# Optimization experiments

Hardware: AMD Instinct MI355X
Metric: run time of the kernel (lower is better)

## Reference

```python
import jax, jax.numpy as jnp
import numpy as np

EPS = 1e-5
NUM_HEADS = 8


def _conv_transpose_3x3_s2(x, w):
    # x: [B,Cin,H,W], w: [Cin,Cout,3,3] (torch ConvTranspose2d layout), stride 2, no padding
    # output spatial = (H-1)*2 + 3 = 2H+1
    return jax.lax.conv_transpose(
        x, w, strides=(2, 2), padding='VALID',
        dimension_numbers=('NCHW', 'IOHW', 'NCHW'))


def setup_inputs() -> dict:
    key = jax.random.key(0)
    ks = jax.random.split(key, 8)
    B, C, H, W = 4, 256, 32, 32
    Co, Dk, Dv = 128, 64, 64
    s = 0.05
    return {
        'x': jax.random.normal(ks[0], (B, C, H, W), jnp.float32),
        'gamma': jnp.ones((C,), jnp.float32),
        'beta': jnp.zeros((C,), jnp.float32),
        'running_mean': jax.random.normal(ks[1], (C,), jnp.float32) * 0.1,
        'running_var': jax.random.uniform(ks[2], (C,), jnp.float32, 0.5, 1.5),
        'w_sc': jax.random.normal(ks[3], (C, Co, 3, 3), jnp.float32) * s,
        'w_q': jax.random.normal(ks[4], (C, Dk, 3, 3), jnp.float32) * s,
        'w_k': jax.random.normal(ks[5], (Dk, C), jnp.float32) * s,
        'w_v': jax.random.normal(ks[6], (Dv, C), jnp.float32) * s,
        'w_o': jax.random.normal(ks[7], (Co, Dv), jnp.float32) * s,
    }


def reference(x, gamma, beta, running_mean, running_var, w_sc, w_q, w_k, w_v, w_o):
    B, C, H, W = x.shape
    h = NUM_HEADS
    # BatchNorm (inference, running stats) + ReLU, shared by both branches
    inv = jax.lax.rsqrt(running_var + EPS)
    xn = (x - running_mean[None, :, None, None]) * (gamma * inv)[None, :, None, None] \
         + beta[None, :, None, None]
    xr = jax.nn.relu(xn)

    # Shortcut: ConvTranspose2d(C->Co, 3, stride 2) -> [B,Co,2H+1,2W+1]
    shortcut = _conv_transpose_3x3_s2(xr, w_sc)

    # Attention branch ('UP'): query upsampled via ConvTranspose, k/v 1x1 at low res
    q = _conv_transpose_3x3_s2(xr, w_q)              # [B,Dk,Hu,Wu]
    k = jnp.einsum('dc,bchw->bdhw', w_k, xr)         # [B,Dk,H,W]
    v = jnp.einsum('dc,bchw->bdhw', w_v, xr)         # [B,Dv,H,W]
    Hu, Wu = q.shape[2], q.shape[3]
    Nq, Nk = Hu * Wu, H * W
    Dk, Dv = q.shape[1], v.shape[1]
    dk = Dk // h
    qh = q.reshape(B, h, dk, Nq)
    kh = k.reshape(B, h, dk, Nk)
    vh = v.reshape(B, h, Dv // h, Nk)
    scores = jnp.einsum('bhdq,bhdk->bhqk', qh, kh) / jnp.sqrt(jnp.float32(dk))
    attn = jax.nn.softmax(scores, axis=-1)           # use_softmax=True
    out = jnp.einsum('bhqk,bhdk->bhdq', attn, vh)    # [B,h,dv,Nq]
    out = out.reshape(B, Dv, Hu, Wu)
    out = jnp.einsum('od,bdhw->bohw', w_o, out)      # 1x1 output projection -> Co

    return shortcut + out
```

## Files before the change

### kernel.cpp

```cpp
#include <hip/hip_runtime.h>

typedef unsigned short u16;
typedef unsigned int u32;

typedef float f4 __attribute__((ext_vector_type(4)));
typedef short s8v __attribute__((ext_vector_type(8)));
typedef u16 us8 __attribute__((ext_vector_type(8)));
typedef _Float16 h4 __attribute__((ext_vector_type(4)));
typedef __fp16 g2 __attribute__((ext_vector_type(2)));

__device__ __forceinline__ u16 f2bf(float x){ u32 b=__float_as_uint(x); b += 0x7FFFu + ((b>>16)&1u); return (u16)(b>>16); }
__device__ __forceinline__ u16 f2h(float x){ union{_Float16 h; u16 u;} c; c.h=(_Float16)x; return c.u; }

#define O_XRT  4096u
#define O_WPT  (O_XRT + 2367488u)
#define O_QH   (O_WPT + 884736u)
#define O_KT   (O_QH  + 2163200u)
#define O_V    (O_KT  + 524288u)
#define O_ATT  (O_V   + 524288u)
#define O_WKV  (O_ATT + 2163200u)
#define O_WO2  (O_WKV + 65536u)

__global__ __launch_bounds__(256) void k_prep(
    const float* __restrict__ x, const float* __restrict__ gamma, const float* __restrict__ beta,
    const float* __restrict__ mean, const float* __restrict__ var,
    const float* __restrict__ w_sc, const float* __restrict__ w_q,
    const float* __restrict__ w_k, const float* __restrict__ w_v, const float* __restrict__ w_o,
    u16* __restrict__ xrTp, u16* __restrict__ wpt,
    u16* __restrict__ wkv, u16* __restrict__ wo2)
{
  __shared__ float SS[128], SH[128];
  __shared__ __align__(16) u16 T[32*136];
  int bi = blockIdx.x, tid = threadIdx.x;
  if (bi < 256) {
    int b = bi >> 6, pt = (bi >> 1) & 31, ch = bi & 1;
    int pix0 = pt*32, c0 = ch*128;
    if (tid < 128) {
      int c = c0 + tid;
      float s = gamma[c]*rsqrtf(var[c] + 1e-5f);
      SS[tid] = s; SH[tid] = beta[c] - mean[c]*s;
    }
    __syncthreads();
    int pix_l = tid & 31, c_l = tid >> 5;
    #pragma unroll 4
    for (int it = 0; it < 16; ++it) {
      int cl = it*8 + c_l;
      float v = x[(((size_t)(b*256 + c0 + cl))<<10) + pix0 + pix_l];
      T[pix_l*136 + cl] = f2bf(fmaxf(v*SS[cl] + SH[cl], 0.f));
    }
    __syncthreads();
    int pix_r = tid >> 3, j = tid & 7;
    us8 v0 = *(const us8*)(T + pix_r*136 + j*8);
    us8 v1 = *(const us8*)(T + pix_r*136 + 64 + j*8);
    u16* dst = xrTp + (((size_t)(b*1156 + (pt+1)*34 + 1 + pix_r))<<8) + c0;
    *(us8*)(dst + j*8) = v0;
    *(us8*)(dst + 64 + j*8) = v1;
    return;
  }
  int wid = (bi - 256)*256 + tid;
  if (wid < 442368) {
    int c, m, ky, kx; float val;
    if (wid < 294912) {
      c = wid / 1152; int r = wid - c*1152; m = r / 9; int t9 = r - m*9; ky = t9/3; kx = t9 - ky*3;
      val = w_sc[wid];
    } else {
      int i2 = wid - 294912;
      c = i2 / 576; int r = i2 - c*576; m = r / 9; int t9 = r - m*9; ky = t9/3; kx = t9 - ky*3;
      val = w_q[i2] * 0.51007023f;
      m += 128;
    }
    int py = (ky==1) ? 1 : 0; int dy = (ky==0) ? 1 : 0;
    int px = (kx==1) ? 1 : 0; int dx = (kx==0) ? 1 : 0;
    int cls = py*2 + px;
    int tt, KP, base;
    if (cls==0){ tt = dy*2+dx; KP=1024; base=0; }
    else if (cls==1){ tt = dy; KP=512; base=196608; }
    else if (cls==2){ tt = dx; KP=512; base=294912; }
    else { tt = 0; KP=256; base=393216; }
    wpt[base + m*KP + tt*256 + c] = f2bf(val);
  } else if (wid < 475136) {
    int i = wid - 442368; int m = i >> 8, c = i & 255;
    float vv = (m < 64) ? w_k[m*256 + c] : w_v[(m-64)*256 + c];
    wkv[m*256 + c] = f2bf(vv);
  } else if (wid < 483328) {
    int i = wid - 475136;
    wo2[i] = f2bf(w_o[i]);
  } else if (wid < 500224) {
    int i = wid - 483328;
    int b = i / 4224; int r = i - b*4224;
    int hp = r >> 5, j = r & 31;
    int p;
    if (hp < 34) p = hp;
    else if (hp < 68) p = 33*34 + (hp - 34);
    else if (hp < 100) p = (hp - 68 + 1)*34;
    else p = (hp - 100 + 1)*34 + 33;
    *(us8*)(xrTp + (((size_t)(b*1156 + p))<<8) + j*8) = (us8)0;
  }
}

template<int PY,int PX,int TT>
__device__ __forceinline__ void conv_cls(
    const u16* __restrict__ xrTp, const u16* __restrict__ wcls,
    float* __restrict__ outF, u16* __restrict__ qh,
    int mb, int nb, u16* Blds)
{
  constexpr int Hy = 33 - PY, Wx = 33 - PX;
  constexpr int NC = 4*Hy*Wx;
  constexpr int KP = TT*256;
  constexpr int NKT = KP/64;
  int tid = threadIdx.x;
  int lane = tid & 63, wv = tid >> 6, quad = lane >> 4, c15 = lane & 15;
  int sn = tid >> 2, sg = tid & 3;
  int n_g = nb*64 + sn;
  int ncl = n_g < NC ? n_g : NC-1;
  int bb = ncl/(Hy*Wx); int rem = ncl - bb*(Hy*Wx); int yq = rem/Wx; int xq = rem - yq*Wx;
  const u16* bsrc = xrTp + (((size_t)(bb*1156 + (yq+1)*34 + xq+1))<<8) + sg*16;
  f4 acc[4];
  #pragma unroll
  for (int i=0;i<4;i++) acc[i] = (f4){0.f,0.f,0.f,0.f};
  const u16* arow = wcls + (size_t)(mb*64 + wv*16 + c15)*KP + quad*8;
  auto loadB = [&](int kt, us8& v0, us8& v1) {
    int tt = kt >> 2, c0 = (kt & 3)*64;
    int dy, dx;
    if (TT==4){ dy = tt>>1; dx = tt&1; }
    else if (TT==2){ if (PX==1){ dy=tt; dx=0; } else { dy=0; dx=tt; } }
    else { dy=0; dx=0; }
    const u16* p = bsrc - (((dy*34+dx))<<8) + c0;
    v0 = *(const us8*)p;
    v1 = *(const us8*)(p+8);
  };
  us8 cv0, cv1; loadB(0, cv0, cv1);
  int pb = 0;
  for (int kt = 0; kt < NKT; ++kt) {
    u16* Bw = Blds + pb*4608;
    *(us8*)(Bw + sn*72 + sg*16) = cv0;
    *(us8*)(Bw + sn*72 + sg*16 + 8) = cv1;
    __syncthreads();
    if (kt + 1 < NKT) loadB(kt+1, cv0, cv1);
    s8v a0 = *(const s8v*)(arow + kt*64);
    s8v a1 = *(const s8v*)(arow + kt*64 + 32);
    #pragma unroll
    for (int t4=0;t4<4;t4++) {
      const u16* br = Blds + pb*4608 + (t4*16 + c15)*72 + quad*8;
      s8v bf0 = *(const s8v*)br;
      s8v bf1 = *(const s8v*)(br + 32);
      acc[t4] = __builtin_amdgcn_mfma_f32_16x16x32_bf16(a0, bf0, acc[t4], 0, 0, 0);
      acc[t4] = __builtin_amdgcn_mfma_f32_16x16x32_bf16(a1, bf1, acc[t4], 0, 0, 0);
    }
    pb ^= 1;
  }
  #pragma unroll
  for (int t4=0;t4<4;t4++) {
    int n2 = nb*64 + t4*16 + c15;
    if (n2 < NC) {
      int bb2 = n2/(Hy*Wx); int rem2 = n2 - bb2*(Hy*Wx); int yq2 = rem2/Wx; int xq2 = rem2 - yq2*Wx;
      int pix = (2*yq2 + PY)*65 + (2*xq2 + PX);
      if (mb < 2) {
        int mrow = mb*64 + wv*16 + quad*4;
        #pragma unroll
        for (int rg=0; rg<4; rg++)
          outF[(size_t)(bb2*128 + mrow + rg)*4225 + pix] = acc[t4][rg];
      } else {
        int dv = wv*16 + quad*4;
        u16 pk[4];
        #pragma unroll
        for (int rg=0; rg<4; rg++) pk[rg] = f2h(acc[t4][rg]);
        *(uint2*)(qh + (((size_t)(bb2*4225 + pix))<<6) + dv) = *(uint2*)pk;
      }
    }
  }
}

__global__ __launch_bounds__(256) void k_conv(
    const u16* __restrict__ xrTp, const u16* __restrict__ wpt, const u16* __restrict__ wkv,
    float* __restrict__ outF, u16* __restrict__ qh,
    u16* __restrict__ kT, u16* __restrict__ vbuf)
{
  __shared__ __align__(16) u16 Blds[2*4608];
  int bi = blockIdx.x;
  if (bi < 795) {
    int mb = bi % 3, cy = bi / 3;
    if (cy < 69)       conv_cls<0,0,4>(xrTp, wpt,          outF, qh, mb, cy,     Blds);
    else if (cy < 135) conv_cls<0,1,2>(xrTp, wpt + 196608, outF, qh, mb, cy-69,  Blds);
    else if (cy < 201) conv_cls<1,0,2>(xrTp, wpt + 294912, outF, qh, mb, cy-135, Blds);
    else               conv_cls<1,1,1>(xrTp, wpt + 393216, outF, qh, mb, cy-201, Blds);
    return;
  }
  int t = bi - 795;
  int mb = t & 1, nb = t >> 1;
  int tid = threadIdx.x;
  int lane = tid & 63, wv = tid >> 6, quad = lane >> 4, c15 = lane & 15;
  int sn = tid >> 2, sg = tid & 3;
  int n_g = nb*64 + sn;
  int b0 = n_g >> 10, pix0 = n_g & 1023, y0 = pix0 >> 5, x0 = pix0 & 31;
  const u16* bsrc = xrTp + (((size_t)(b0*1156 + (y0+1)*34 + x0+1))<<8) + sg*16;
  f4 acc[4];
  #pragma unroll
  for (int i=0;i<4;i++) acc[i] = (f4){0.f,0.f,0.f,0.f};
  const u16* arow = wkv + (size_t)(mb*64 + wv*16 + c15)*256 + quad*8;
  us8 cv0 = *(const us8*)bsrc, cv1 = *(const us8*)(bsrc + 8);
  int pb = 0;
  for (int kt = 0; kt < 4; ++kt) {
    u16* Bw = Blds + pb*4608;
    *(us8*)(Bw + sn*72 + sg*16) = cv0;
    *(us8*)(Bw + sn*72 + sg*16 + 8) = cv1;
    __syncthreads();
    if (kt < 3) { cv0 = *(const us8*)(bsrc + (kt+1)*64); cv1 = *(const us8*)(bsrc + (kt+1)*64 + 8); }
    s8v a0 = *(const s8v*)(arow + kt*64);
    s8v a1 = *(const s8v*)(arow + kt*64 + 32);
    #pragma unroll
    for (int t4=0;t4<4;t4++) {
      const u16* br = Blds + pb*4608 + (t4*16 + c15)*72 + quad*8;
      s8v bf0 = *(const s8v*)br;
      s8v bf1 = *(const s8v*)(br + 32);
      acc[t4] = __builtin_amdgcn_mfma_f32_16x16x32_bf16(a0, bf0, acc[t4], 0, 0, 0);
      acc[t4] = __builtin_amdgcn_mfma_f32_16x16x32_bf16(a1, bf1, acc[t4], 0, 0, 0);
    }
    pb ^= 1;
  }
  int ml = wv*16 + quad*4;
  #pragma unroll
  for (int t4=0;t4<4;t4++) {
    int n2 = nb*64 + t4*16 + c15;
    int b = n2 >> 10, pix = n2 & 1023;
    if (mb == 0) {
      int h = ml >> 3, d0 = ml & 7;
      u16 pk[4];
      #pragma unroll
      for (int rg=0; rg<4; rg++) pk[rg] = f2h(acc[t4][rg]);
      *(uint2*)(kT + ((size_t)(b*8+h)<<13) + pix*8 + d0) = *(uint2*)pk;
    } else {
      #pragma unroll
      for (int rg=0; rg<4; rg++)
        vbuf[(((size_t)(b*64 + ml + rg))<<10) + pix] = f2h(acc[t4][rg]);
    }
  }
}

__global__ __launch_bounds__(256) void k_attn(
    const u16* __restrict__ qh, const u16* __restrict__ kT, const u16* __restrict__ vbuf,
    u16* __restrict__ attT)
{
  __shared__ __align__(16) u16 KL[8192];
  __shared__ __align__(16) u16 VL[9*1032];
  int qt = blockIdx.x, bh = blockIdx.y;
  int b = bh >> 3, h = bh & 7;
  int tid = threadIdx.x, lane = tid & 63, wv = tid >> 6, quad = lane >> 4, c15 = lane & 15;
  {
    const uint4* kg = (const uint4*)(kT + ((size_t)bh << 13));
    for (int i = tid; i < 1024; i += 256) ((uint4*)KL)[i] = kg[i];
    const u16* vg = vbuf + ((size_t)(b*64 + h*8) << 10);
    for (int i = tid; i < 1024; i += 256) {
      int dv = i >> 7, k8 = (i & 127) << 3;
      *(uint4*)(VL + dv*1032 + k8) = *(const uint4*)(vg + (dv<<10) + k8);
    }
    if (tid < 129) {
      us8 ones;
      #pragma unroll
      for (int i=0;i<8;i++) ones[i] = 0x3C00;
      *(us8*)(VL + 8*1032 + tid*8) = ones;
    }
  }
  __syncthreads();
  int q0 = qt*128 + wv*32 + c15;
  int q1 = q0 + 16;
  int qa = q0 < 4224 ? q0 : 4224;
  int qb = q1 < 4224 ? q1 : 4224;
  uint2 t0 = *(const uint2*)(qh + (((size_t)(b*4225 + qa))<<6) + h*8 + (quad&1)*4);
  uint2 t1 = *(const uint2*)(qh + (((size_t)(b*4225 + qb))<<6) + h*8 + (quad&1)*4);
  h4 bq0 = quad < 2 ? *(h4*)&t0 : (h4)(_Float16)0.f;
  h4 bq1 = quad < 2 ? *(h4*)&t1 : (h4)(_Float16)0.f;
  const u16* klb = KL + c15*8 + (quad&1)*4;
  int vr = c15 > 8 ? 8 : c15;
  const u16* vlb = VL + vr*1032 + quad*4;
  const f4 zf = {0.f,0.f,0.f,0.f};
  f4 O0 = {0.f,0.f,0.f,0.f}, O1 = {0.f,0.f,0.f,0.f};
  union HU { uint2 u; h4 h; };
  #pragma unroll 8
  for (int kt=0; kt<64; ++kt) {
    h4 ak = *(const h4*)(klb + kt*128);
    h4 av = *(const h4*)(vlb + kt*16);
    f4 s0 = __builtin_amdgcn_mfma_f32_16x16x16f16(ak, bq0, zf, 0, 0, 0);
    f4 s1 = __builtin_amdgcn_mfma_f32_16x16x16f16(ak, bq1, zf, 0, 0, 0);
    g2 p0l = __builtin_amdgcn_cvt_pkrtz(__builtin_amdgcn_exp2f(s0[0]), __builtin_amdgcn_exp2f(s0[1]));
    g2 p0h = __builtin_amdgcn_cvt_pkrtz(__builtin_amdgcn_exp2f(s0[2]), __builtin_amdgcn_exp2f(s0[3]));
    g2 p1l = __builtin_amdgcn_cvt_pkrtz(__builtin_amdgcn_exp2f(s1[0]), __builtin_amdgcn_exp2f(s1[1]));
    g2 p1h = __builtin_amdgcn_cvt_pkrtz(__builtin_amdgcn_exp2f(s1[2]), __builtin_amdgcn_exp2f(s1[3]));
    HU u0; u0.u.x = __builtin_bit_cast(u32, p0l); u0.u.y = __builtin_bit_cast(u32, p0h);
    HU u1; u1.u.x = __builtin_bit_cast(u32, p1l); u1.u.y = __builtin_bit_cast(u32, p1h);
    O0 = __builtin_amdgcn_mfma_f32_16x16x16f16(av, u0.h, O0, 0, 0, 0);
    O1 = __builtin_amdgcn_mfma_f32_16x16x16f16(av, u1.h, O1, 0, 0, 0);
  }
  float l0 = __shfl(O0[0], 32 + c15, 64);
  float l1 = __shfl(O1[0], 32 + c15, 64);
  float r0 = __builtin_amdgcn_rcpf(l0);
  float r1 = __builtin_amdgcn_rcpf(l1);
  if (quad < 2) {
    if (q0 < 4225) {
      u16 pk[4];
      #pragma unroll
      for (int rg=0;rg<4;rg++) pk[rg] = f2bf(O0[rg]*r0);
      *(uint2*)(attT + (((size_t)(b*4225 + q0))<<6) + h*8 + quad*4) = *(uint2*)pk;
    }
    if (q1 < 4225) {
      u16 pk[4];
      #pragma unroll
      for (int rg=0;rg<4;rg++) pk[rg] = f2bf(O1[rg]*r1);
      *(uint2*)(attT + (((size_t)(b*4225 + q1))<<6) + h*8 + quad*4) = *(uint2*)pk;
    }
  }
}

__global__ __launch_bounds__(256) void k_proj(
    const u16* __restrict__ attT, const u16* __restrict__ wo2, float* __restrict__ outF)
{
  int nbi = blockIdx.x, b = blockIdx.y;
  int tid = threadIdx.x;
  int lane = tid & 63, wv = tid >> 6, quad = lane >> 4, c15 = lane & 15;
  f4 acc[2][4];
  #pragma unroll
  for (int am=0;am<2;am++)
    #pragma unroll
    for (int i=0;i<4;i++) acc[am][i] = (f4){0.f,0.f,0.f,0.f};
  #pragma unroll
  for (int kt = 0; kt < 2; ++kt) {
    s8v a0 = *(const s8v*)(wo2 + (size_t)(wv*32 + c15)*64 + kt*32 + quad*8);
    s8v a1 = *(const s8v*)(wo2 + (size_t)(wv*32 + 16 + c15)*64 + kt*32 + quad*8);
    #pragma unroll
    for (int t4=0;t4<4;t4++) {
      int n = nbi*64 + t4*16 + c15;
      int nc = n < 4224 ? n : 4224;
      s8v bf = *(const s8v*)(attT + (((size_t)(b*4225 + nc))<<6) + kt*32 + quad*8);
      acc[0][t4] = __builtin_amdgcn_mfma_f32_16x16x32_bf16(a0, bf, acc[0][t4], 0, 0, 0);
      acc[1][t4] = __builtin_amdgcn_mfma_f32_16x16x32_bf16(a1, bf, acc[1][t4], 0, 0, 0);
    }
  }
  #pragma unroll
  for (int am=0;am<2;am++) {
    int mrow = wv*32 + am*16 + quad*4;
    #pragma unroll
    for (int t4=0;t4<4;t4++) {
      int n2 = nbi*64 + t4*16 + c15;
      if (n2 < 4225) {
        float* op = outF + (size_t)(b*128 + mrow)*4225 + n2;
        #pragma unroll
        for (int rg=0; rg<4; rg++) op[(size_t)rg*4225] += acc[am][t4][rg];
      }
    }
  }
}

extern "C" void kernel_launch(void* const* d_in, const int* in_sizes, int n_in,
                              void* d_out, int out_size, void* d_ws, size_t ws_size,
                              hipStream_t stream) {
  const float* x     = (const float*)d_in[0];
  const float* gamma = (const float*)d_in[1];
  const float* beta  = (const float*)d_in[2];
  const float* mean  = (const float*)d_in[3];
  const float* var   = (const float*)d_in[4];
  const float* w_sc  = (const float*)d_in[5];
  const float* w_q   = (const float*)d_in[6];
  const float* w_k   = (const float*)d_in[7];
  const float* w_v   = (const float*)d_in[8];
  const float* w_o   = (const float*)d_in[9];
  char* ws = (char*)d_ws;
  u16*   xrTp = (u16*)(ws + O_XRT);
  u16*   wpt  = (u16*)(ws + O_WPT);
  u16*   qhb  = (u16*)(ws + O_QH);
  u16*   kT   = (u16*)(ws + O_KT);
  u16*   vbuf = (u16*)(ws + O_V);
  u16*   attT = (u16*)(ws + O_ATT);
  u16*   wkv  = (u16*)(ws + O_WKV);
  u16*   wo2  = (u16*)(ws + O_WO2);
  float* outF = (float*)d_out;

  k_prep<<<2211, 256, 0, stream>>>(x, gamma, beta, mean, var, w_sc, w_q, w_k, w_v, w_o,
                                   xrTp, wpt, wkv, wo2);
  k_conv<<<923, 256, 0, stream>>>(xrTp, wpt, wkv, outF, qhb, kT, vbuf);
  k_attn<<<dim3(34, 32), 256, 0, stream>>>(qhb, kT, vbuf, attT);
  k_proj<<<dim3(67, 4), 256, 0, stream>>>(attT, wo2, outF);
}
```

Measured before the change: 135.5 us.

## Fuse four kernels into persistent megakernel with global atomic barriers

Replaces the prep, conv, attention and projection launches with a single persistent kernel of 1024 blocks that loops over work units and separates stages with atomic-counter grid barriers, after a memset resets the counters. The goal is to remove launch gaps and the tail between kernels. In exchange it adds spin-wait barrier cost, needs all 1024 blocks co-resident (launch bounds of 4 blocks per CU) or it deadlocks, and may lower per-stage occupancy and parallelism, for example in the attention stage, which has more work units than blocks.

```diff
diff --git a/kernel.cpp b/kernel.cpp
--- a/kernel.cpp
+++ b/kernel.cpp
@@ -21,81 +21,17 @@
 #define O_WKV  (O_ATT + 2163200u)
 #define O_WO2  (O_WKV + 65536u)
 
-__global__ __launch_bounds__(256) void k_prep(
-    const float* __restrict__ x, const float* __restrict__ gamma, const float* __restrict__ beta,
-    const float* __restrict__ mean, const float* __restrict__ var,
-    const float* __restrict__ w_sc, const float* __restrict__ w_q,
-    const float* __restrict__ w_k, const float* __restrict__ w_v, const float* __restrict__ w_o,
-    u16* __restrict__ xrTp, u16* __restrict__ wpt,
-    u16* __restrict__ wkv, u16* __restrict__ wo2)
-{
-  __shared__ float SS[128], SH[128];
-  __shared__ __align__(16) u16 T[32*136];
-  int bi = blockIdx.x, tid = threadIdx.x;
-  if (bi < 256) {
-    int b = bi >> 6, pt = (bi >> 1) & 31, ch = bi & 1;
-    int pix0 = pt*32, c0 = ch*128;
-    if (tid < 128) {
-      int c = c0 + tid;
-      float s = gamma[c]*rsqrtf(var[c] + 1e-5f);
-      SS[tid] = s; SH[tid] = beta[c] - mean[c]*s;
-    }
-    __syncthreads();
-    int pix_l = tid & 31, c_l = tid >> 5;
-    #pragma unroll 4
-    for (int it = 0; it < 16; ++it) {
-      int cl = it*8 + c_l;
-      float v = x[(((size_t)(b*256 + c0 + cl))<<10) + pix0 + pix_l];
-      T[pix_l*136 + cl] = f2bf(fmaxf(v*SS[cl] + SH[cl], 0.f));
-    }
-    __syncthreads();
-    int pix_r = tid >> 3, j = tid & 7;
-    us8 v0 = *(const us8*)(T + pix_r*136 + j*8);
-    us8 v1 = *(const us8*)(T + pix_r*136 + 64 + j*8);
-    u16* dst = xrTp + (((size_t)(b*1156 + (pt+1)*34 + 1 + pix_r))<<8) + c0;
-    *(us8*)(dst + j*8) = v0;
-    *(us8*)(dst + 64 + j*8) = v1;
-    return;
-  }
-  int wid = (bi - 256)*256 + tid;
-  if (wid < 442368) {
-    int c, m, ky, kx; float val;
-    if (wid < 294912) {
-      c = wid / 1152; int r = wid - c*1152; m = r / 9; int t9 = r - m*9; ky = t9/3; kx = t9 - ky*3;
-      val = w_sc[wid];
-    } else {
-      int i2 = wid - 294912;
-      c = i2 / 576; int r = i2 - c*576; m = r / 9; int t9 = r - m*9; ky = t9/3; kx = t9 - ky*3;
-      val = w_q[i2] * 0.51007023f;
-      m += 128;
-    }
-    int py = (ky==1) ? 1 : 0; int dy = (ky==0) ? 1 : 0;
-    int px = (kx==1) ? 1 : 0; int dx = (kx==0) ? 1 : 0;
-    int cls = py*2 + px;
-    int tt, KP, base;
-    if (cls==0){ tt = dy*2+dx; KP=1024; base=0; }
-    else if (cls==1){ tt = dy; KP=512; base=196608; }
-    else if (cls==2){ tt = dx; KP=512; base=294912; }
-    else { tt = 0; KP=256; base=393216; }
-    wpt[base + m*KP + tt*256 + c] = f2bf(val);
-  } else if (wid < 475136) {
-    int i = wid - 442368; int m = i >> 8, c = i & 255;
-    float vv = (m < 64) ? w_k[m*256 + c] : w_v[(m-64)*256 + c];
-    wkv[m*256 + c] = f2bf(vv);
-  } else if (wid < 483328) {
-    int i = wid - 475136;
-    wo2[i] = f2bf(w_o[i]);
-  } else if (wid < 500224) {
-    int i = wid - 483328;
-    int b = i / 4224; int r = i - b*4224;
-    int hp = r >> 5, j = r & 31;
-    int p;
-    if (hp < 34) p = hp;
-    else if (hp < 68) p = 33*34 + (hp - 34);
-    else if (hp < 100) p = (hp - 68 + 1)*34;
-    else p = (hp - 100 + 1)*34 + 33;
-    *(us8*)(xrTp + (((size_t)(b*1156 + p))<<8) + j*8) = (us8)0;
-  }
+#define NBLK 1024
+
+__device__ __forceinline__ void gbar(u32* c) {
+  __syncthreads();
+  if (threadIdx.x == 0) {
+    __threadfence();
+    atomicAdd(c, 1u);
+    while (atomicAdd(c, 0u) < (u32)NBLK) __builtin_amdgcn_s_sleep(4);
+    __threadfence();
+  }
+  __syncthreads();
 }
 
 template<int PY,int PX,int TT>
@@ -171,180 +107,268 @@
   }
 }
 
-__global__ __launch_bounds__(256) void k_conv(
-    const u16* __restrict__ xrTp, const u16* __restrict__ wpt, const u16* __restrict__ wkv,
-    float* __restrict__ outF, u16* __restrict__ qh,
-    u16* __restrict__ kT, u16* __restrict__ vbuf)
+__global__ __launch_bounds__(256, 4) void k_mega(
+    const float* __restrict__ x, const float* __restrict__ gamma, const float* __restrict__ beta,
+    const float* __restrict__ mean, const float* __restrict__ var,
+    const float* __restrict__ w_sc, const float* __restrict__ w_q,
+    const float* __restrict__ w_k, const float* __restrict__ w_v, const float* __restrict__ w_o,
+    char* __restrict__ ws, float* __restrict__ outF)
 {
-  __shared__ __align__(16) u16 Blds[2*4608];
-  int bi = blockIdx.x;
-  if (bi < 795) {
-    int mb = bi % 3, cy = bi / 3;
-    if (cy < 69)       conv_cls<0,0,4>(xrTp, wpt,          outF, qh, mb, cy,     Blds);
-    else if (cy < 135) conv_cls<0,1,2>(xrTp, wpt + 196608, outF, qh, mb, cy-69,  Blds);
-    else if (cy < 201) conv_cls<1,0,2>(xrTp, wpt + 294912, outF, qh, mb, cy-135, Blds);
-    else               conv_cls<1,1,1>(xrTp, wpt + 393216, outF, qh, mb, cy-201, Blds);
-    return;
-  }
-  int t = bi - 795;
-  int mb = t & 1, nb = t >> 1;
-  int tid = threadIdx.x;
-  int lane = tid & 63, wv = tid >> 6, quad = lane >> 4, c15 = lane & 15;
-  int sn = tid >> 2, sg = tid & 3;
-  int n_g = nb*64 + sn;
-  int b0 = n_g >> 10, pix0 = n_g & 1023, y0 = pix0 >> 5, x0 = pix0 & 31;
-  const u16* bsrc = xrTp + (((size_t)(b0*1156 + (y0+1)*34 + x0+1))<<8) + sg*16;
-  f4 acc[4];
-  #pragma unroll
-  for (int i=0;i<4;i++) acc[i] = (f4){0.f,0.f,0.f,0.f};
-  const u16* arow = wkv + (size_t)(mb*64 + wv*16 + c15)*256 + quad*8;
-  us8 cv0 = *(const us8*)bsrc, cv1 = *(const us8*)(bsrc + 8);
-  int pb = 0;
-  for (int kt = 0; kt < 4; ++kt) {
-    u16* Bw = Blds + pb*4608;
-    *(us8*)(Bw + sn*72 + sg*16) = cv0;
-    *(us8*)(Bw + sn*72 + sg*16 + 8) = cv1;
-    __syncthreads();
-    if (kt < 3) { cv0 = *(const us8*)(bsrc + (kt+1)*64); cv1 = *(const us8*)(bsrc + (kt+1)*64 + 8); }
-    s8v a0 = *(const s8v*)(arow + kt*64);
-    s8v a1 = *(const s8v*)(arow + kt*64 + 32);
-    #pragma unroll
-    for (int t4=0;t4<4;t4++) {
-      const u16* br = Blds + pb*4608 + (t4*16 + c15)*72 + quad*8;
-      s8v bf0 = *(const s8v*)br;
-      s8v bf1 = *(const s8v*)(br + 32);
-      acc[t4] = __builtin_amdgcn_mfma_f32_16x16x32_bf16(a0, bf0, acc[t4], 0, 0, 0);
-      acc[t4] = __builtin_amdgcn_mfma_f32_16x16x32_bf16(a1, bf1, acc[t4], 0, 0, 0);
-    }
-    pb ^= 1;
-  }
-  int ml = wv*16 + quad*4;
-  #pragma unroll
-  for (int t4=0;t4<4;t4++) {
-    int n2 = nb*64 + t4*16 + c15;
-    int b = n2 >> 10, pix = n2 & 1023;
-    if (mb == 0) {
-      int h = ml >> 3, d0 = ml & 7;
-      u16 pk[4];
+  __shared__ __align__(16) char SM[35072];
+  u32* bar = (u32*)ws;
+  u16* xrTp = (u16*)(ws + O_XRT);
+  u16* wpt  = (u16*)(ws + O_WPT);
+  u16* qh   = (u16*)(ws + O_QH);
+  u16* kT   = (u16*)(ws + O_KT);
+  u16* vbuf = (u16*)(ws + O_V);
+  u16* attT = (u16*)(ws + O_ATT);
+  u16* wkv  = (u16*)(ws + O_WKV);
+  u16* wo2  = (u16*)(ws + O_WO2);
+  int bid = blockIdx.x, tid = threadIdx.x;
+
+  {
+    float* SS = (float*)SM; float* SH = SS + 64; u16* T = (u16*)(SH + 64);
+    for (int u = bid; u < 2466; u += NBLK) {
+      if (u < 512) {
+        int b = u >> 7, pt = (u >> 2) & 31, ch = u & 3;
+        int pix0 = pt*32, c0 = ch*64;
+        if (tid < 64) {
+          int c = c0 + tid;
+          float s = gamma[c]*rsqrtf(var[c] + 1e-5f);
+          SS[tid] = s; SH[tid] = beta[c] - mean[c]*s;
+        }
+        __syncthreads();
+        int pix_l = tid & 31, c_l = tid >> 5;
+        #pragma unroll
+        for (int it = 0; it < 8; ++it) {
+          int cl = it*8 + c_l;
+          float v = x[(((size_t)(b*256 + c0 + cl))<<10) + pix0 + pix_l];
+          T[pix_l*72 + cl] = f2bf(fmaxf(v*SS[cl] + SH[cl], 0.f));
+        }
+        __syncthreads();
+        int pix_r = tid >> 3, j = tid & 7;
+        us8 v0 = *(const us8*)(T + pix_r*72 + j*8);
+        u16* dst = xrTp + (((size_t)(b*1156 + (pt+1)*34 + 1 + pix_r))<<8) + c0;
+        *(us8*)(dst + j*8) = v0;
+        __syncthreads();
+      } else {
+        int wid = (u - 512)*256 + tid;
+        if (wid < 442368) {
+          int c, m, ky, kx; float val;
+          if (wid < 294912) {
+            c = wid / 1152; int r = wid - c*1152; m = r / 9; int t9 = r - m*9; ky = t9/3; kx = t9 - ky*3;
+            val = w_sc[wid];
+          } else {
+            int i2 = wid - 294912;
+            c = i2 / 576; int r = i2 - c*576; m = r / 9; int t9 = r - m*9; ky = t9/3; kx = t9 - ky*3;
+            val = w_q[i2] * 0.51007023f;
+            m += 128;
+          }
+          int py = (ky==1) ? 1 : 0; int dy = (ky==0) ? 1 : 0;
+          int px = (kx==1) ? 1 : 0; int dx = (kx==0) ? 1 : 0;
+          int cls = py*2 + px;
+          int tt, KP, base;
+          if (cls==0){ tt = dy*2+dx; KP=1024; base=0; }
+          else if (cls==1){ tt = dy; KP=512; base=196608; }
+          else if (cls==2){ tt = dx; KP=512; base=294912; }
+          else { tt = 0; KP=256; base=393216; }
+          wpt[base + m*KP + tt*256 + c] = f2bf(val);
+        } else if (wid < 475136) {
+          int i = wid - 442368; int m = i >> 8, c = i & 255;
+          float vv = (m < 64) ? w_k[m*256 + c] : w_v[(m-64)*256 + c];
+          wkv[m*256 + c] = f2bf(vv);
+        } else if (wid < 483328) {
+          int i = wid - 475136;
+          wo2[i] = f2bf(w_o[i]);
+        } else if (wid < 500224) {
+          int i = wid - 483328;
+          int b = i / 4224; int r = i - b*4224;
+          int hp = r >> 5, j = r & 31;
+          int p;
+          if (hp < 34) p = hp;
+          else if (hp < 68) p = 33*34 + (hp - 34);
+          else if (hp < 100) p = (hp - 68 + 1)*34;
+          else p = (hp - 100 + 1)*34 + 33;
+          *(us8*)(xrTp + (((size_t)(b*1156 + p))<<8) + j*8) = (us8)0;
+        }
+      }
+    }
+  }
+  gbar(bar + 0);
+
+  {
+    u16* Blds = (u16*)SM;
+    for (int u = bid; u < 923; u += NBLK) {
+      if (u < 795) {
+        int mb = u % 3, cy = u / 3;
+        if (cy < 69)       conv_cls<0,0,4>(xrTp, wpt,          outF, qh, mb, cy,     Blds);
+        else if (cy < 135) conv_cls<0,1,2>(xrTp, wpt + 196608, outF, qh, mb, cy-69,  Blds);
+        else if (cy < 201) conv_cls<1,0,2>(xrTp, wpt + 294912, outF, qh, mb, cy-135, Blds);
+        else               conv_cls<1,1,1>(xrTp, wpt + 393216, outF, qh, mb, cy-201, Blds);
+      } else {
+        int t = u - 795;
+        int mb = t & 1, nb = t >> 1;
+        int lane = tid & 63, wv = tid >> 6, quad = lane >> 4, c15 = lane & 15;
+        int sn = tid >> 2, sg = tid & 3;
+        int n_g = nb*64 + sn;
+        int b0 = n_g >> 10, pix0 = n_g & 1023, y0 = pix0 >> 5, x0 = pix0 & 31;
+        const u16* bsrc = xrTp + (((size_t)(b0*1156 + (y0+1)*34 + x0+1))<<8) + sg*16;
+        f4 acc[4];
+        #pragma unroll
+        for (int i=0;i<4;i++) acc[i] = (f4){0.f,0.f,0.f,0.f};
+        const u16* arow = wkv + (size_t)(mb*64 + wv*16 + c15)*256 + quad*8;
+        us8 cv0 = *(const us8*)bsrc, cv1 = *(const us8*)(bsrc + 8);
+        int pb = 0;
+        for (int kt = 0; kt < 4; ++kt) {
+          u16* Bw = Blds + pb*4608;
+          *(us8*)(Bw + sn*72 + sg*16) = cv0;
+          *(us8*)(Bw + sn*72 + sg*16 + 8) = cv1;
+          __syncthreads();
+          if (kt < 3) { cv0 = *(const us8*)(bsrc + (kt+1)*64); cv1 = *(const us8*)(bsrc + (kt+1)*64 + 8); }
+          s8v a0 = *(const s8v*)(arow + kt*64);
+          s8v a1 = *(const s8v*)(arow + kt*64 + 32);
+          #pragma unroll
+          for (int t4=0;t4<4;t4++) {
+            const u16* br = Blds + pb*4608 + (t4*16 + c15)*72 + quad*8;
+            s8v bf0 = *(const s8v*)br;
+            s8v bf1 = *(const s8v*)(br + 32);
+            acc[t4] = __builtin_amdgcn_mfma_f32_16x16x32_bf16(a0, bf0, acc[t4], 0, 0, 0);
+            acc[t4] = __builtin_amdgcn_mfma_f32_16x16x32_bf16(a1, bf1, acc[t4], 0, 0, 0);
+          }
+          pb ^= 1;
+        }
+        int ml = wv*16 + quad*4;
+        #pragma unroll
+        for (int t4=0;t4<4;t4++) {
+          int n2 = nb*64 + t4*16 + c15;
+          int b = n2 >> 10, pix = n2 & 1023;
+          if (mb == 0) {
+            int h = ml >> 3, d0 = ml & 7;
+            u16 pk[4];
+            #pragma unroll
+            for (int rg=0; rg<4; rg++) pk[rg] = f2h(acc[t4][rg]);
+            *(uint2*)(kT + ((size_t)(b*8+h)<<13) + pix*8 + d0) = *(uint2*)pk;
+          } else {
+            #pragma unroll
+            for (int rg=0; rg<4; rg++)
+              vbuf[(((size_t)(b*64 + ml + rg))<<10) + pix] = f2h(acc[t4][rg]);
+          }
+        }
+      }
+      __syncthreads();
+    }
+  }
+  gbar(bar + 1);
+
+  {
+    u16* KL = (u16*)SM;
+    u16* VL = KL + 8192;
+    int lane = tid & 63, wv = tid >> 6, quad = lane >> 4, c15 = lane & 15;
+    for (int u = bid; u < 1088; u += NBLK) {
+      int qt = u % 34, bh = u / 34;
+      int b = bh >> 3, h = bh & 7;
+      {
+        const uint4* kg = (const uint4*)(kT + ((size_t)bh << 13));
+        for (int i = tid; i < 1024; i += 256) ((uint4*)KL)[i] = kg[i];
+        const u16* vg = vbuf + ((size_t)(b*64 + h*8) << 10);
+        for (int i = tid; i < 1024; i += 256) {
+          int dv = i >> 7, k8 = (i & 127) << 3;
+          *(uint4*)(VL + dv*1032 + k8) = *(const uint4*)(vg + (dv<<10) + k8);
+        }
+        if (tid < 129) {
+          us8 ones;
+          #pragma unroll
+          for (int i=0;i<8;i++) ones[i] = 0x3C00;
+          *(us8*)(VL + 8*1032 + tid*8) = ones;
+        }
+      }
+      __syncthreads();
+      int q0 = qt*128 + wv*32 + c15;
+      int q1 = q0 + 16;
+      int qa = q0 < 4224 ? q0 : 4224;
+      int qb = q1 < 4224 ? q1 : 4224;
+      uint2 t0 = *(const uint2*)(qh + (((size_t)(b*4225 + qa))<<6) + h*8 + (quad&1)*4);
+      uint2 t1 = *(const uint2*)(qh + (((size_t)(b*4225 + qb))<<6) + h*8 + (quad&1)*4);
+      h4 bq0 = quad < 2 ? *(h4*)&t0 : (h4)(_Float16)0.f;
+      h4 bq1 = quad < 2 ? *(h4*)&t1 : (h4)(_Float16)0.f;
+      const u16* klb = KL + c15*8 + (quad&1)*4;
+      int vr = c15 > 8 ? 8 : c15;
+      const u16* vlb = VL + vr*1032 + quad*4;
+      const f4 zf = {0.f,0.f,0.f,0.f};
+      f4 O0 = {0.f,0.f,0.f,0.f}, O1 = {0.f,0.f,0.f,0.f};
+      union HU { uint2 u; h4 h; };
+      #pragma unroll 8
+      for (int kt=0; kt<64; ++kt) {
+        h4 ak = *(const h4*)(klb + kt*128);
+        h4 av = *(const h4*)(vlb + kt*16);
+        f4 s0 = __builtin_amdgcn_mfma_f32_16x16x16f16(ak, bq0, zf, 0, 0, 0);
+        f4 s1 = __builtin_amdgcn_mfma_f32_16x16x16f16(ak, bq1, zf, 0, 0, 0);
+        g2 p0l = __builtin_amdgcn_cvt_pkrtz(__builtin_amdgcn_exp2f(s0[0]), __builtin_amdgcn_exp2f(s0[1]));
+        g2 p0h = __builtin_amdgcn_cvt_pkrtz(__builtin_amdgcn_exp2f(s0[2]), __builtin_amdgcn_exp2f(s0[3]));
+        g2 p1l = __builtin_amdgcn_cvt_pkrtz(__builtin_amdgcn_exp2f(s1[0]), __builtin_amdgcn_exp2f(s1[1]));
+        g2 p1h = __builtin_amdgcn_cvt_pkrtz(__builtin_amdgcn_exp2f(s1[2]), __builtin_amdgcn_exp2f(s1[3]));
+        HU u0; u0.u.x = __builtin_bit_cast(u32, p0l); u0.u.y = __builtin_bit_cast(u32, p0h);
+        HU u1; u1.u.x = __builtin_bit_cast(u32, p1l); u1.u.y = __builtin_bit_cast(u32, p1h);
+        O0 = __builtin_amdgcn_mfma_f32_16x16x16f16(av, u0.h, O0, 0, 0, 0);
+        O1 = __builtin_amdgcn_mfma_f32_16x16x16f16(av, u1.h, O1, 0, 0, 0);
+      }
+      float l0 = __shfl(O0[0], 32 + c15, 64);
+      float l1 = __shfl(O1[0], 32 + c15, 64);
+      float r0 = __builtin_amdgcn_rcpf(l0);
+      float r1 = __builtin_amdgcn_rcpf(l1);
+      if (quad < 2) {
+        if (q0 < 4225) {
+          u16 pk[4];
+          #pragma unroll
+          for (int rg=0;rg<4;rg++) pk[rg] = f2bf(O0[rg]*r0);
+          *(uint2*)(attT + (((size_t)(b*4225 + q0))<<6) + h*8 + quad*4) = *(uint2*)pk;
+        }
+        if (q1 < 4225) {
+          u16 pk[4];
+          #pragma unroll
+          for (int rg=0;rg<4;rg++) pk[rg] = f2bf(O1[rg]*r1);
+          *(uint2*)(attT + (((size_t)(b*4225 + q1))<<6) + h*8 + quad*4) = *(uint2*)pk;
+        }
+      }
+      __syncthreads();
+    }
+  }
+  gbar(bar + 2);
+
+  {
+    int lane = tid & 63, wv = tid >> 6, quad = lane >> 4, c15 = lane & 15;
+    for (int u = bid; u < 268; u += NBLK) {
+      int nbi = u % 67, b = u / 67;
+      f4 acc[2][4];
       #pragma unroll
-      for (int rg=0; rg<4; rg++) pk[rg] = f2h(acc[t4][rg]);
-      *(uint2*)(kT + ((size_t)(b*8+h)<<13) + pix*8 + d0) = *(uint2*)pk;
-    } else {
+      for (int am=0;am<2;am++)
+        #pragma unroll
+        for (int i=0;i<4;i++) acc[am][i] = (f4){0.f,0.f,0.f,0.f};
       #pragma unroll
-      for (int rg=0; rg<4; rg++)
-        vbuf[(((size_t)(b*64 + ml + rg))<<10) + pix] = f2h(acc[t4][rg]);
-    }
-  }
-}
-
-__global__ __launch_bounds__(256) void k_attn(
-    const u16* __restrict__ qh, const u16* __restrict__ kT, const u16* __restrict__ vbuf,
-    u16* __restrict__ attT)
-{
-  __shared__ __align__(16) u16 KL[8192];
-  __shared__ __align__(16) u16 VL[9*1032];
-  int qt = blockIdx.x, bh = blockIdx.y;
-  int b = bh >> 3, h = bh & 7;
-  int tid = threadIdx.x, lane = tid & 63, wv = tid >> 6, quad = lane >> 4, c15 = lane & 15;
-  {
-    const uint4* kg = (const uint4*)(kT + ((size_t)bh << 13));
-    for (int i = tid; i < 1024; i += 256) ((uint4*)KL)[i] = kg[i];
-    const u16* vg = vbuf + ((size_t)(b*64 + h*8) << 10);
-    for (int i = tid; i < 1024; i += 256) {
-      int dv = i >> 7, k8 = (i & 127) << 3;
-      *(uint4*)(VL + dv*1032 + k8) = *(const uint4*)(vg + (dv<<10) + k8);
-    }
-    if (tid < 129) {
-      us8 ones;
+      for (int kt = 0; kt < 2; ++kt) {
+        s8v a0 = *(const s8v*)(wo2 + (size_t)(wv*32 + c15)*64 + kt*32 + quad*8);
+        s8v a1 = *(const s8v*)(wo2 + (size_t)(wv*32 + 16 + c15)*64 + kt*32 + quad*8);
+        #pragma unroll
+        for (int t4=0;t4<4;t4++) {
+          int n = nbi*64 + t4*16 + c15;
+          int nc = n < 4224 ? n : 4224;
+          s8v bf = *(const s8v*)(attT + (((size_t)(b*4225 + nc))<<6) + kt*32 + quad*8);
+          acc[0][t4] = __builtin_amdgcn_mfma_f32_16x16x32_bf16(a0, bf, acc[0][t4], 0, 0, 0);
+          acc[1][t4] = __builtin_amdgcn_mfma_f32_16x16x32_bf16(a1, bf, acc[1][t4], 0, 0, 0);
+        }
+      }
       #pragma unroll
-      for (int i=0;i<8;i++) ones[i] = 0x3C00;
-      *(us8*)(VL + 8*1032 + tid*8) = ones;
-    }
-  }
-  __syncthreads();
-  int q0 = qt*128 + wv*32 + c15;
-  int q1 = q0 + 16;
-  int qa = q0 < 4224 ? q0 : 4224;
-  int qb = q1 < 4224 ? q1 : 4224;
-  uint2 t0 = *(const uint2*)(qh + (((size_t)(b*4225 + qa))<<6) + h*8 + (quad&1)*4);
-  uint2 t1 = *(const uint2*)(qh + (((size_t)(b*4225 + qb))<<6) + h*8 + (quad&1)*4);
-  h4 bq0 = quad < 2 ? *(h4*)&t0 : (h4)(_Float16)0.f;
-  h4 bq1 = quad < 2 ? *(h4*)&t1 : (h4)(_Float16)0.f;
-  const u16* klb = KL + c15*8 + (quad&1)*4;
-  int vr = c15 > 8 ? 8 : c15;
-  const u16* vlb = VL + vr*1032 + quad*4;
-  const f4 zf = {0.f,0.f,0.f,0.f};
-  f4 O0 = {0.f,0.f,0.f,0.f}, O1 = {0.f,0.f,0.f,0.f};
-  union HU { uint2 u; h4 h; };
-  #pragma unroll 8
-  for (int kt=0; kt<64; ++kt) {
-    h4 ak = *(const h4*)(klb + kt*128);
-    h4 av = *(const h4*)(vlb + kt*16);
-    f4 s0 = __builtin_amdgcn_mfma_f32_16x16x16f16(ak, bq0, zf, 0, 0, 0);
-    f4 s1 = __builtin_amdgcn_mfma_f32_16x16x16f16(ak, bq1, zf, 0, 0, 0);
-    g2 p0l = __builtin_amdgcn_cvt_pkrtz(__builtin_amdgcn_exp2f(s0[0]), __builtin_amdgcn_exp2f(s0[1]));
-    g2 p0h = __builtin_amdgcn_cvt_pkrtz(__builtin_amdgcn_exp2f(s0[2]), __builtin_amdgcn_exp2f(s0[3]));
-    g2 p1l = __builtin_amdgcn_cvt_pkrtz(__builtin_amdgcn_exp2f(s1[0]), __builtin_amdgcn_exp2f(s1[1]));
-    g2 p1h = __builtin_amdgcn_cvt_pkrtz(__builtin_amdgcn_exp2f(s1[2]), __builtin_amdgcn_exp2f(s1[3]));
-    HU u0; u0.u.x = __builtin_bit_cast(u32, p0l); u0.u.y = __builtin_bit_cast(u32, p0h);
-    HU u1; u1.u.x = __builtin_bit_cast(u32, p1l); u1.u.y = __builtin_bit_cast(u32, p1h);
-    O0 = __builtin_amdgcn_mfma_f32_16x16x16f16(av, u0.h, O0, 0, 0, 0);
-    O1 = __builtin_amdgcn_mfma_f32_16x16x16f16(av, u1.h, O1, 0, 0, 0);
-  }
-  float l0 = __shfl(O0[0], 32 + c15, 64);
-  float l1 = __shfl(O1[0], 32 + c15, 64);
-  float r0 = __builtin_amdgcn_rcpf(l0);
-  float r1 = __builtin_amdgcn_rcpf(l1);
-  if (quad < 2) {
-    if (q0 < 4225) {
-      u16 pk[4];
-      #pragma unroll
-      for (int rg=0;rg<4;rg++) pk[rg] = f2bf(O0[rg]*r0);
-      *(uint2*)(attT + (((size_t)(b*4225 + q0))<<6) + h*8 + quad*4) = *(uint2*)pk;
-    }
-    if (q1 < 4225) {
-      u16 pk[4];
-      #pragma unroll
-      for (int rg=0;rg<4;rg++) pk[rg] = f2bf(O1[rg]*r1);
-      *(uint2*)(attT + (((size_t)(b*4225 + q1))<<6) + h*8 + quad*4) = *(uint2*)pk;
-    }
-  }
-}
-
-__global__ __launch_bounds__(256) void k_proj(
-    const u16* __restrict__ attT, const u16* __restrict__ wo2, float* __restrict__ outF)
-{
-  int nbi = blockIdx.x, b = blockIdx.y;
-  int tid = threadIdx.x;
-  int lane = tid & 63, wv = tid >> 6, quad = lane >> 4, c15 = lane & 15;
-  f4 acc[2][4];
-  #pragma unroll
-  for (int am=0;am<2;am++)
-    #pragma unroll
-    for (int i=0;i<4;i++) acc[am][i] = (f4){0.f,0.f,0.f,0.f};
-  #pragma unroll
-  for (int kt = 0; kt < 2; ++kt) {
-    s8v a0 = *(const s8v*)(wo2 + (size_t)(wv*32 + c15)*64 + kt*32 + quad*8);
-    s8v a1 = *(const s8v*)(wo2 + (size_t)(wv*32 + 16 + c15)*64 + kt*32 + quad*8);
-    #pragma unroll
-    for (int t4=0;t4<4;t4++) {
-      int n = nbi*64 + t4*16 + c15;
-      int nc = n < 4224 ? n : 4224;
-      s8v bf = *(const s8v*)(attT + (((size_t)(b*4225 + nc))<<6) + kt*32 + quad*8);
-      acc[0][t4] = __builtin_amdgcn_mfma_f32_16x16x32_bf16(a0, bf, acc[0][t4], 0, 0, 0);
-      acc[1][t4] = __builtin_amdgcn_mfma_f32_16x16x32_bf16(a1, bf, acc[1][t4], 0, 0, 0);
-    }
-  }
-  #pragma unroll
-  for (int am=0;am<2;am++) {
-    int mrow = wv*32 + am*16 + quad*4;
-    #pragma unroll
-    for (int t4=0;t4<4;t4++) {
-      int n2 = nbi*64 + t4*16 + c15;
-      if (n2 < 4225) {
-        float* op = outF + (size_t)(b*128 + mrow)*4225 + n2;
-        #pragma unroll
-        for (int rg=0; rg<4; rg++) op[(size_t)rg*4225] += acc[am][t4][rg];
+      for (int am=0;am<2;am++) {
+        int mrow = wv*32 + am*16 + quad*4;
+        #pragma unroll
+        for (int t4=0;t4<4;t4++) {
+          int n2 = nbi*64 + t4*16 + c15;
+          if (n2 < 4225) {
+            float* op = outF + (size_t)(b*128 + mrow)*4225 + n2;
+            #pragma unroll
+            for (int rg=0; rg<4; rg++) op[(size_t)rg*4225] += acc[am][t4][rg];
+          }
+        }
       }
     }
   }
@@ -364,19 +388,9 @@
   const float* w_v   = (const float*)d_in[8];
   const float* w_o   = (const float*)d_in[9];
   char* ws = (char*)d_ws;
-  u16*   xrTp = (u16*)(ws + O_XRT);
-  u16*   wpt  = (u16*)(ws + O_WPT);
-  u16*   qhb  = (u16*)(ws + O_QH);
-  u16*   kT   = (u16*)(ws + O_KT);
-  u16*   vbuf = (u16*)(ws + O_V);
-  u16*   attT = (u16*)(ws + O_ATT);
-  u16*   wkv  = (u16*)(ws + O_WKV);
-  u16*   wo2  = (u16*)(ws + O_WO2);
   float* outF = (float*)d_out;
 
-  k_prep<<<2211, 256, 0, stream>>>(x, gamma, beta, mean, var, w_sc, w_q, w_k, w_v, w_o,
-                                   xrTp, wpt, wkv, wo2);
-  k_conv<<<923, 256, 0, stream>>>(xrTp, wpt, wkv, outF, qhb, kT, vbuf);
-  k_attn<<<dim3(34, 32), 256, 0, stream>>>(qhb, kT, vbuf, attT);
-  k_proj<<<dim3(67, 4), 256, 0, stream>>>(attT, wo2, outF);
+  hipMemsetAsync(ws, 0, 256, stream);
+  k_mega<<<NBLK, 256, 0, stream>>>(x, gamma, beta, mean, var, w_sc, w_q, w_k, w_v, w_o,
+                                   ws, outF);
 }
```

After: 464.7 us. 243% more time.
